# Kernel optimization log

Measured on AMD Instinct MI355X. Metric: run time of the kernel, lower is better.

## Reference

```python
import jax, jax.numpy as jnp
import numpy as np

B, L, E, H, D = 2, 4096, 512, 8, 64
DIL, WIN, CAUSAL = 2, 256, True
HID = 2048  # mlp_ratio * embed_dim
EPS = 1e-5


def _layernorm(x, g, b):
    mu = jnp.mean(x, axis=-1, keepdims=True)
    var = jnp.var(x, axis=-1, keepdims=True)
    return (x - mu) * jax.lax.rsqrt(var + EPS) * g + b


def _dilated_mask(Lq):
    i = jnp.arange(Lq)[:, None]
    j = jnp.arange(Lq)[None, :]
    d = i - j
    allowed = (d % DIL) == 0
    allowed &= jnp.abs(d) <= WIN
    if CAUSAL:
        allowed &= j <= i
    return allowed  # [L, L] bool


def setup_inputs() -> dict:
    key = jax.random.key(0)
    ks = jax.random.split(key, 5)
    s = 0.02
    return {
        "x": jax.random.normal(ks[0], (B, L, E), jnp.float32),
        "ln1_g": jnp.ones((E,), jnp.float32),
        "ln1_b": jnp.zeros((E,), jnp.float32),
        "qkv_w": jax.random.normal(ks[1], (E, 3 * E), jnp.float32) * s,
        "qkv_b": jnp.zeros((3 * E,), jnp.float32),
        "out_w": jax.random.normal(ks[2], (E, E), jnp.float32) * s,
        "out_b": jnp.zeros((E,), jnp.float32),
        "ln2_g": jnp.ones((E,), jnp.float32),
        "ln2_b": jnp.zeros((E,), jnp.float32),
        "w1": jax.random.normal(ks[3], (E, HID), jnp.float32) * s,
        "b1": jnp.zeros((HID,), jnp.float32),
        "w2": jax.random.normal(ks[4], (HID, E), jnp.float32) * s,
        "b2": jnp.zeros((E,), jnp.float32),
    }


def reference(x, ln1_g, ln1_b, qkv_w, qkv_b, out_w, out_b, ln2_g, ln2_b, w1, b1, w2, b2):
    b, l, e = x.shape
    # --- attention sublayer (pre-norm) ---
    h = _layernorm(x, ln1_g, ln1_b)
    qkv = h @ qkv_w + qkv_b                      # [B, L, 3E]
    q, k, v = jnp.split(qkv, 3, axis=-1)
    q = q.reshape(b, l, H, D).transpose(0, 2, 1, 3)  # [B, H, L, D]
    k = k.reshape(b, l, H, D).transpose(0, 2, 1, 3)
    v = v.reshape(b, l, H, D).transpose(0, 2, 1, 3)
    scores = jnp.einsum("bhqd,bhkd->bhqk", q, k) / jnp.sqrt(jnp.asarray(D, x.dtype))
    mask = _dilated_mask(l)                      # [L, L] bool, dilation+window+causal
    scores = jnp.where(mask, scores, jnp.finfo(scores.dtype).min)
    attn = jax.nn.softmax(scores, axis=-1)
    o = jnp.einsum("bhqk,bhkd->bhqd", attn, v)   # [B, H, L, D]
    o = o.transpose(0, 2, 1, 3).reshape(b, l, e)
    x = x + (o @ out_w + out_b)                  # dropout p=0
    # --- FFN sublayer (pre-norm) ---
    h2 = _layernorm(x, ln2_g, ln2_b)
    f = jax.nn.gelu(h2 @ w1 + b1, approximate=False) @ w2 + b2
    return x + f
```

## Files before the change

kernel.cpp:

```cpp
#include <hip/hip_runtime.h>
#include <math.h>

typedef unsigned char u8;
typedef unsigned short u16;
typedef unsigned int u32;
typedef __attribute__((ext_vector_type(4))) float f32x4;
typedef __attribute__((ext_vector_type(8))) short short8;

#define B_DIM 2
#define L_SEQ 4096
#define E_DIM 512
#define NH 8
#define HD 64
#define HID_DIM 2048
#define BL (B_DIM * L_SEQ)

__device__ __forceinline__ float bf2f(u16 u) {
    union { u32 i; float f; } v; v.i = ((u32)u) << 16; return v.f;
}
__device__ __forceinline__ u16 f2bf(float f) {
    union { float f; u32 i; } v; v.f = f;
    u32 r = v.i + 0x7fffu + ((v.i >> 16) & 1u);
    return (u16)(r >> 16);
}
__device__ __forceinline__ u32 pk2_fp8(float a, float b) {
    return (u32)__builtin_amdgcn_cvt_pk_fp8_f32(a, b, 0, false);
}
__device__ __forceinline__ u8 f2fp8(float a) { return (u8)(pk2_fp8(a, a) & 0xffu); }
__device__ __forceinline__ float gelu_f(float v) {
    float y = fminf(0.7978845608f * (v + 0.044715f * v * v * v), 15.f);
    float t = __expf(2.f * y);
    return v * (t / (t + 1.f));
}

#define GLOAD_LDS16(gp, lp) __builtin_amdgcn_global_load_lds( \
    (const __attribute__((address_space(1))) void*)(gp),      \
    (__attribute__((address_space(3))) void*)(lp), 16, 0, 0)

template<int VM> __device__ __forceinline__ void waitvm() {
    asm volatile("s_waitcnt vmcnt(%0)" :: "n"(VM) : "memory");
}

__global__ __launch_bounds__(256) void wconv_f8(const float* __restrict__ in,
                                                u8* __restrict__ out, int Kd, int Nd) {
    __shared__ u8 t[64][96];
    const int k0 = blockIdx.y * 64, n0 = blockIdx.x * 64;
    const int tid = threadIdx.x;
    const int col4 = tid & 15, rowb = tid >> 4;
#pragma unroll
    for (int i = 0; i < 4; ++i) {
        const int k = rowb + i * 16;
        const float4 v = *(const float4*)(in + (size_t)(k0 + k) * Nd + n0 + col4 * 4);
        const u32 p01 = pk2_fp8(v.x * 32.f, v.y * 32.f);
        const u32 p23 = pk2_fp8(v.z * 32.f, v.w * 32.f);
        t[col4 * 4 + 0][k] = (u8)(p01 & 0xff);
        t[col4 * 4 + 1][k] = (u8)((p01 >> 8) & 0xff);
        t[col4 * 4 + 2][k] = (u8)(p23 & 0xff);
        t[col4 * 4 + 3][k] = (u8)((p23 >> 8) & 0xff);
    }
    __syncthreads();
    const int n = tid >> 2, ch = tid & 3;
    u8* dst = out + (size_t)(n0 + n) * Kd + k0 + ch * 16;
    *(short8*)dst = *(const short8*)&t[n][ch * 16];
}

__global__ __launch_bounds__(256) void ln_f8(const float* __restrict__ x,
                                             const float* __restrict__ g,
                                             const float* __restrict__ b,
                                             u8* __restrict__ out) {
    const int row = blockIdx.x * 4 + (threadIdx.x >> 6);
    const int lane = threadIdx.x & 63;
    const float4* xr = (const float4*)(x + (size_t)row * E_DIM);
    const float4 v0 = xr[lane];
    const float4 v1 = xr[lane + 64];
    float s  = v0.x + v0.y + v0.z + v0.w + v1.x + v1.y + v1.z + v1.w;
    float s2 = v0.x*v0.x + v0.y*v0.y + v0.z*v0.z + v0.w*v0.w
             + v1.x*v1.x + v1.y*v1.y + v1.z*v1.z + v1.w*v1.w;
#pragma unroll
    for (int off = 32; off > 0; off >>= 1) {
        s  += __shfl_xor(s, off);
        s2 += __shfl_xor(s2, off);
    }
    const float mu = s * (1.f / E_DIM);
    const float rs = rsqrtf(s2 * (1.f / E_DIM) - mu * mu + 1e-5f);
    const float4 g0 = ((const float4*)g)[lane], g1 = ((const float4*)g)[lane + 64];
    const float4 b0 = ((const float4*)b)[lane], b1 = ((const float4*)b)[lane + 64];
    const float a0 = (v0.x - mu) * rs * g0.x + b0.x;
    const float a1 = (v0.y - mu) * rs * g0.y + b0.y;
    const float a2 = (v0.z - mu) * rs * g0.z + b0.z;
    const float a3 = (v0.w - mu) * rs * g0.w + b0.w;
    const float a4 = (v1.x - mu) * rs * g1.x + b1.x;
    const float a5 = (v1.y - mu) * rs * g1.y + b1.y;
    const float a6 = (v1.z - mu) * rs * g1.z + b1.z;
    const float a7 = (v1.w - mu) * rs * g1.w + b1.w;
    u32* orow = (u32*)(out + (size_t)row * E_DIM);
    orow[lane]      = pk2_fp8(a0, a1) | (pk2_fp8(a2, a3) << 16);
    orow[lane + 64] = pk2_fp8(a4, a5) | (pk2_fp8(a6, a7) << 16);
}

template<int K_T, int BN_T, int OUT, bool RES, bool GELU>
__global__ __launch_bounds__(512) void gemm_f8(const u8* __restrict__ A,
                                               const u8* __restrict__ Bt,
                                               const float* __restrict__ bias,
                                               const float* __restrict__ res,
                                               void* __restrict__ Cp,
                                               int M, int N, int nbx) {
    constexpr int K = K_T;
    constexpr int NT = K / 64;
    constexpr int MR = 4;
    constexpr int NR = BN_T / 64;
    constexpr int GA = 8;
    constexpr int GB = BN_T / 16;
    constexpr int LB = GB / 8;
    constexpr int L = 1 + LB;
    constexpr int AKG_S = GA * 256;
    constexpr int BKG_S = GB * 256;
    constexpr int ABYTES = 128 * 64;
    constexpr int BBYTES = BN_T * 64;
    constexpr int TILE = ABYTES + BBYTES;
    __shared__ u8 sb[3 * TILE];
    const int tid = threadIdx.x;
    const int wave = tid >> 6, lane = tid & 63;
    const int wr = wave >> 2, wc = wave & 3;

    const int xcd = blockIdx.x & 7;
    const int q = blockIdx.x >> 3;
    const int bx = q % nbx;
    const int by = (q / nbx) * 8 + xcd;
    const int bm = by * 128, bn = bx * BN_T;

    f32x4 acc[MR][NR];
#pragma unroll
    for (int m = 0; m < MR; ++m)
#pragma unroll
        for (int n = 0; n < NR; ++n) acc[m][n] = 0.f;

    const int lrow = (lane >> 4) * 16 + (lane & 15);

    auto stage = [&](int buf, int t) {
        u8* dst0 = sb + buf * TILE;
        {
            const int kg = wave >> 1, j = wave & 1;
            const u8* src = A + (size_t)(bm + j * 64 + lrow) * K
                            + t * 64 + (kg >> 1) * 32 + (kg & 1) * 16;
            GLOAD_LDS16(src, dst0 + kg * AKG_S + j * 1024);
        }
#pragma unroll
        for (int h = 0; h < LB; ++h) {
            const int i = wave * LB + h;
            const int kg = i / (GB / 4), j = i % (GB / 4);
            const u8* src = Bt + (size_t)(bn + j * 64 + lrow) * K
                            + t * 64 + (kg >> 1) * 32 + (kg & 1) * 16;
            GLOAD_LDS16(src, dst0 + ABYTES + kg * BKG_S + j * 1024);
        }
    };

    auto compute = [&](int buf) {
        const u8* base = sb + buf * TILE;
        const int g = lane >> 4, r = lane & 15;
        const int sub = g >> 1, off8 = (g & 1) * 8;
#pragma unroll
        for (int ks = 0; ks < 2; ++ks) {
            long av[MR], bv[NR];
#pragma unroll
            for (int m = 0; m < MR; ++m)
                av[m] = *(const long*)(base + (ks * 2 + sub) * AKG_S
                                       + (wr * 4 + m) * 256 + r * 16 + off8);
#pragma unroll
            for (int n = 0; n < NR; ++n)
                bv[n] = *(const long*)(base + ABYTES + (ks * 2 + sub) * BKG_S
                                       + (wc * NR + n) * 256 + r * 16 + off8);
            __builtin_amdgcn_s_setprio(1);
#pragma unroll
            for (int m = 0; m < MR; ++m)
#pragma unroll
                for (int n = 0; n < NR; ++n)
                    acc[m][n] = __builtin_amdgcn_mfma_f32_16x16x32_fp8_fp8(av[m], bv[n], acc[m][n], 0, 0, 0);
            __builtin_amdgcn_s_setprio(0);
        }
    };

    stage(0, 0);
    stage(1, 1);
    int sbuf = 2, cbuf = 0;
    for (int t = 0; t < NT - 2; ++t) {
        stage(sbuf, t + 2);
        sbuf = (sbuf == 2) ? 0 : sbuf + 1;
        waitvm<2 * L>();
        __builtin_amdgcn_s_barrier();
        compute(cbuf);
        cbuf = (cbuf == 2) ? 0 : cbuf + 1;
        __builtin_amdgcn_s_barrier();
    }
    waitvm<L>();
    __builtin_amdgcn_s_barrier();
    compute(cbuf);
    cbuf = (cbuf == 2) ? 0 : cbuf + 1;
    __builtin_amdgcn_s_barrier();
    waitvm<0>();
    __builtin_amdgcn_s_barrier();
    compute(cbuf);

    const int ccol = lane & 15;
    const int crow = (lane >> 4) * 4;
#pragma unroll
    for (int n = 0; n < NR; ++n) {
        const int gc = bn + wc * (NR * 16) + n * 16 + ccol;
        const float bi = bias[gc];
#pragma unroll
        for (int m = 0; m < MR; ++m) {
            const int gr0 = bm + wr * 64 + m * 16 + crow;
#pragma unroll
            for (int j = 0; j < 4; ++j) {
                float v = acc[m][n][j] * 0.03125f + bi;
                if (GELU) v = gelu_f(v);
                const size_t idx = (size_t)(gr0 + j) * N + gc;
                if (RES) v += res[idx];
                if (OUT == 0)      ((u16*)Cp)[idx] = f2bf(v);
                else if (OUT == 1) ((float*)Cp)[idx] = v;
                else               ((u8*)Cp)[idx] = f2fp8(v);
            }
        }
    }
}

__global__ __launch_bounds__(256) void attn_mfma(const u16* __restrict__ qkv,
                                                 u8* __restrict__ o) {
    __shared__ u16 K_lds[32 * 64];
    __shared__ u16 V_lds[32 * 64];
    const int tid = threadIdx.x;
    const int w = tid >> 6, lane = tid & 63;
    const int g = lane >> 4, q = lane & 15;
    const int qt = blockIdx.x, bph = blockIdx.y;
    const int b = bph >> 4, p = (bph >> 3) & 1, h = bph & 7;
    const int q0 = qt * 64;

    const size_t rowstride = 3 * E_DIM;
    const u16* qbase = qkv + (size_t)b * L_SEQ * rowstride + h * HD;

    const int qmin = q0 + w * 16, qmax = qmin + 15;
    const int qs_lane = qmin + q;
    const int qi = 2 * qs_lane + p;

    short8 qfrag[2];
    qfrag[0] = *(const short8*)(qbase + (size_t)qi * rowstride + g * 8);
    qfrag[1] = *(const short8*)(qbase + (size_t)qi * rowstride + 32 + g * 8);

    f32x4 oacc[4];
#pragma unroll
    for (int dt = 0; dt < 4; ++dt) oacc[dt] = 0.f;
    float m = -1e30f, l = 0.f;

    for (int s = 0; s < 6; ++s) {
        const int ks0 = q0 - 128 + 32 * s;
        if (ks0 >= 0) {
            const int r = 8 * w + (lane >> 3);
            const int gr = lane & 7;
            const size_t krow = (size_t)(2 * (ks0 + r) + p) * rowstride;
            const u16* ksrc = qbase + krow + E_DIM + 8 * (gr ^ (r & 7));
            const u16* vsrc = qbase + krow + 2 * E_DIM + 8 * gr;
            GLOAD_LDS16(ksrc, &K_lds[w * 512]);
            GLOAD_LDS16(vsrc, &V_lds[w * 512]);
        }
        __syncthreads();
        const bool active = (ks0 >= 0) && (ks0 <= qmax) && (ks0 + 31 >= qmin - 128);
        if (active) {
            f32x4 st[2];
            st[0] = 0.f; st[1] = 0.f;
#pragma unroll
            for (int t = 0; t < 2; ++t) {
#pragma unroll
                for (int c = 0; c < 2; ++c) {
                    const int kk = t * 16 + q;
                    const int gs = (c * 4 + g) ^ (kk & 7);
                    short8 kf = *(const short8*)&K_lds[kk * 64 + gs * 8];
                    st[t] = __builtin_amdgcn_mfma_f32_16x16x32_bf16(kf, qfrag[c], st[t], 0, 0, 0);
                }
            }
            float sv[2][4];
            float bm = -3.0e38f;
#pragma unroll
            for (int t = 0; t < 2; ++t)
#pragma unroll
                for (int j = 0; j < 4; ++j) {
                    const int kk = ks0 + t * 16 + 4 * g + j;
                    float x = st[t][j] * 0.125f;
                    const bool ok = (kk <= qs_lane) && (qs_lane - kk <= 128);
                    x = ok ? x : -3.0e38f;
                    sv[t][j] = x;
                    bm = fmaxf(bm, x);
                }
            bm = fmaxf(bm, __shfl_xor(bm, 16));
            bm = fmaxf(bm, __shfl_xor(bm, 32));
            const float mn = fmaxf(m, bm);
            const float sc = __expf(m - mn);
            m = mn;
            float rs = 0.f;
            u32 pk[2][2];
#pragma unroll
            for (int t = 0; t < 2; ++t) {
                const float e0 = __expf(sv[t][0] - mn), e1 = __expf(sv[t][1] - mn);
                const float e2 = __expf(sv[t][2] - mn), e3 = __expf(sv[t][3] - mn);
                rs += (e0 + e1) + (e2 + e3);
                pk[t][0] = (u32)f2bf(e0) | ((u32)f2bf(e1) << 16);
                pk[t][1] = (u32)f2bf(e2) | ((u32)f2bf(e3) << 16);
            }
            rs += __shfl_xor(rs, 16);
            rs += __shfl_xor(rs, 32);
            l = l * sc + rs;
#pragma unroll
            for (int dt = 0; dt < 4; ++dt) oacc[dt] *= sc;
            union { u32 w4[4]; short8 s8; } bfr;
#pragma unroll
            for (int r = 0; r < 4; ++r) {
                const int src = (((g << 1) + (r >> 1)) & 3) * 16 + q;
                const int w0 = __shfl((int)pk[0][r & 1], src);
                const int w1 = __shfl((int)pk[1][r & 1], src);
                bfr.w4[r] = (g & 2) ? (u32)w1 : (u32)w0;
            }
#pragma unroll
            for (int dt = 0; dt < 4; ++dt) {
                union { u16 h8[8]; short8 s8; } vf;
#pragma unroll
                for (int e = 0; e < 8; ++e)
                    vf.h8[e] = V_lds[(8 * g + e) * 64 + dt * 16 + q];
                oacc[dt] = __builtin_amdgcn_mfma_f32_16x16x32_bf16(vf.s8, bfr.s8, oacc[dt], 0, 0, 0);
            }
        }
        __syncthreads();
    }
    const float inv = 1.f / l;
    u8* obase = o + ((size_t)(b * L_SEQ) + (size_t)qi) * E_DIM + h * HD;
#pragma unroll
    for (int dt = 0; dt < 4; ++dt) {
        const u32 pw = pk2_fp8(oacc[dt][0] * inv, oacc[dt][1] * inv)
                     | (pk2_fp8(oacc[dt][2] * inv, oacc[dt][3] * inv) << 16);
        *(u32*)(obase + dt * 16 + 4 * g) = pw;
    }
}

extern "C" void kernel_launch(void* const* d_in, const int* in_sizes, int n_in,
                              void* d_out, int out_size, void* d_ws, size_t ws_size,
                              hipStream_t stream) {
    const float* x    = (const float*)d_in[0];
    const float* ln1g = (const float*)d_in[1];
    const float* ln1b = (const float*)d_in[2];
    const float* qkvw = (const float*)d_in[3];
    const float* qkvb = (const float*)d_in[4];
    const float* outw = (const float*)d_in[5];
    const float* outb = (const float*)d_in[6];
    const float* ln2g = (const float*)d_in[7];
    const float* ln2b = (const float*)d_in[8];
    const float* w1   = (const float*)d_in[9];
    const float* b1   = (const float*)d_in[10];
    const float* w2   = (const float*)d_in[11];
    const float* b2   = (const float*)d_in[12];
    float* outp = (float*)d_out;

    char* ws = (char*)d_ws;
    size_t off = 0;
    auto alloc = [&](size_t bytes) {
        void* p = ws + off;
        off += (bytes + 255) & ~(size_t)255;
        return p;
    };
    u8*    hbuf  = (u8*)   alloc((size_t)BL * E_DIM);
    u16*   qkvB  = (u16*)  alloc((size_t)BL * 3 * E_DIM * 2);
    u8*    obuf  = (u8*)   alloc((size_t)BL * E_DIM);
    float* x2    = (float*)alloc((size_t)BL * E_DIM * 4);
    u8*    h2    = (u8*)   alloc((size_t)BL * E_DIM);
    u8*    g1    = (u8*)   alloc((size_t)BL * HID_DIM);
    u8*    wqkvT = (u8*)   alloc((size_t)3 * E_DIM * E_DIM);
    u8*    woutT = (u8*)   alloc((size_t)E_DIM * E_DIM);
    u8*    w1T   = (u8*)   alloc((size_t)HID_DIM * E_DIM);
    u8*    w2T   = (u8*)   alloc((size_t)E_DIM * HID_DIM);

    wconv_f8<<<dim3((3 * E_DIM) / 64, E_DIM / 64), 256, 0, stream>>>(qkvw, wqkvT, E_DIM, 3 * E_DIM);
    wconv_f8<<<dim3(E_DIM / 64, E_DIM / 64), 256, 0, stream>>>(outw, woutT, E_DIM, E_DIM);
    wconv_f8<<<dim3(HID_DIM / 64, E_DIM / 64), 256, 0, stream>>>(w1, w1T, E_DIM, HID_DIM);
    wconv_f8<<<dim3(E_DIM / 64, HID_DIM / 64), 256, 0, stream>>>(w2, w2T, HID_DIM, E_DIM);

    ln_f8<<<BL / 4, 256, 0, stream>>>(x, ln1g, ln1b, hbuf);
    gemm_f8<E_DIM, 256, 0, false, false><<<(BL / 128) * 6, 512, 0, stream>>>(
        hbuf, wqkvT, qkvb, nullptr, qkvB, BL, 3 * E_DIM, 6);
    attn_mfma<<<dim3(32, 32), 256, 0, stream>>>(qkvB, obuf);
    gemm_f8<E_DIM, 128, 1, true, false><<<(BL / 128) * 4, 512, 0, stream>>>(
        obuf, woutT, outb, x, x2, BL, E_DIM, 4);
    ln_f8<<<BL / 4, 256, 0, stream>>>(x2, ln2g, ln2b, h2);
    gemm_f8<E_DIM, 256, 2, false, true><<<(BL / 128) * 8, 512, 0, stream>>>(
        h2, w1T, b1, nullptr, g1, BL, HID_DIM, 8);
    gemm_f8<HID_DIM, 128, 1, true, false><<<(BL / 128) * 4, 512, 0, stream>>>(
        g1, w2T, b2, x2, outp, BL, E_DIM, 4);
}
```

Measured before the change: 134.3 us.

## Fuse weight conversion with LN1, store residual in bf16, deepen 128-wide GEMM pipeline

Merges the four weight-conversion launches and the first layernorm into one prep kernel to cut launch overhead. The intermediate residual x2 is stored as bf16 instead of fp32, which halves its write and read traffic in the out-proj GEMM, LN2 and the final GEMM. The GEMMs with 128-wide N tiles use a 4-buffer LDS pipeline with a deeper prefetch instead of 3 buffers. The bf16 residual loses some precision in the skip connection, and the larger LDS footprint may lower occupancy.

```diff
diff --git a/kernel.cpp b/kernel.cpp
--- a/kernel.cpp
+++ b/kernel.cpp
@@ -41,11 +41,57 @@
     asm volatile("s_waitcnt vmcnt(%0)" :: "n"(VM) : "memory");
 }
 
-__global__ __launch_bounds__(256) void wconv_f8(const float* __restrict__ in,
-                                                u8* __restrict__ out, int Kd, int Nd) {
+__global__ __launch_bounds__(256) void prep(const float* __restrict__ qkvw,
+                                            const float* __restrict__ outw,
+                                            const float* __restrict__ w1,
+                                            const float* __restrict__ w2,
+                                            u8* __restrict__ wqkvT, u8* __restrict__ woutT,
+                                            u8* __restrict__ w1T, u8* __restrict__ w2T,
+                                            const float* __restrict__ x,
+                                            const float* __restrict__ g,
+                                            const float* __restrict__ b,
+                                            u8* __restrict__ hbuf) {
     __shared__ u8 t[64][96];
-    const int k0 = blockIdx.y * 64, n0 = blockIdx.x * 64;
+    int bid = blockIdx.x;
     const int tid = threadIdx.x;
+    if (bid < BL / 4) {
+        const int row = bid * 4 + (tid >> 6);
+        const int lane = tid & 63;
+        const float4* xr = (const float4*)(x + (size_t)row * E_DIM);
+        const float4 v0 = xr[lane];
+        const float4 v1 = xr[lane + 64];
+        float s  = v0.x + v0.y + v0.z + v0.w + v1.x + v1.y + v1.z + v1.w;
+        float s2 = v0.x*v0.x + v0.y*v0.y + v0.z*v0.z + v0.w*v0.w
+                 + v1.x*v1.x + v1.y*v1.y + v1.z*v1.z + v1.w*v1.w;
+#pragma unroll
+        for (int off = 32; off > 0; off >>= 1) {
+            s  += __shfl_xor(s, off);
+            s2 += __shfl_xor(s2, off);
+        }
+        const float mu = s * (1.f / E_DIM);
+        const float rs = rsqrtf(s2 * (1.f / E_DIM) - mu * mu + 1e-5f);
+        const float4 g0 = ((const float4*)g)[lane], g1 = ((const float4*)g)[lane + 64];
+        const float4 b0 = ((const float4*)b)[lane], b1 = ((const float4*)b)[lane + 64];
+        const float a0 = (v0.x - mu) * rs * g0.x + b0.x;
+        const float a1 = (v0.y - mu) * rs * g0.y + b0.y;
+        const float a2 = (v0.z - mu) * rs * g0.z + b0.z;
+        const float a3 = (v0.w - mu) * rs * g0.w + b0.w;
+        const float a4 = (v1.x - mu) * rs * g1.x + b1.x;
+        const float a5 = (v1.y - mu) * rs * g1.y + b1.y;
+        const float a6 = (v1.z - mu) * rs * g1.z + b1.z;
+        const float a7 = (v1.w - mu) * rs * g1.w + b1.w;
+        u32* orow = (u32*)(hbuf + (size_t)row * E_DIM);
+        orow[lane]      = pk2_fp8(a0, a1) | (pk2_fp8(a2, a3) << 16);
+        orow[lane + 64] = pk2_fp8(a4, a5) | (pk2_fp8(a6, a7) << 16);
+        return;
+    }
+    bid -= BL / 4;
+    const float* in; u8* out; int Kd, Nd, nbx;
+    if (bid < 192)      {            in = qkvw; out = wqkvT; Kd = E_DIM;   Nd = 3 * E_DIM; nbx = 24; }
+    else if (bid < 256) { bid -= 192; in = outw; out = woutT; Kd = E_DIM;   Nd = E_DIM;     nbx = 8;  }
+    else if (bid < 512) { bid -= 256; in = w1;   out = w1T;   Kd = E_DIM;   Nd = HID_DIM;   nbx = 32; }
+    else                { bid -= 512; in = w2;   out = w2T;   Kd = HID_DIM; Nd = E_DIM;     nbx = 8;  }
+    const int k0 = (bid / nbx) * 64, n0 = (bid % nbx) * 64;
     const int col4 = tid & 15, rowb = tid >> 4;
 #pragma unroll
     for (int i = 0; i < 4; ++i) {
@@ -64,18 +110,19 @@
     *(short8*)dst = *(const short8*)&t[n][ch * 16];
 }
 
-__global__ __launch_bounds__(256) void ln_f8(const float* __restrict__ x,
-                                             const float* __restrict__ g,
-                                             const float* __restrict__ b,
-                                             u8* __restrict__ out) {
+__global__ __launch_bounds__(256) void ln_b(const u16* __restrict__ x,
+                                            const float* __restrict__ g,
+                                            const float* __restrict__ b,
+                                            u8* __restrict__ out) {
     const int row = blockIdx.x * 4 + (threadIdx.x >> 6);
     const int lane = threadIdx.x & 63;
-    const float4* xr = (const float4*)(x + (size_t)row * E_DIM);
-    const float4 v0 = xr[lane];
-    const float4 v1 = xr[lane + 64];
-    float s  = v0.x + v0.y + v0.z + v0.w + v1.x + v1.y + v1.z + v1.w;
-    float s2 = v0.x*v0.x + v0.y*v0.y + v0.z*v0.z + v0.w*v0.w
-             + v1.x*v1.x + v1.y*v1.y + v1.z*v1.z + v1.w*v1.w;
+    const short8 v = *(const short8*)(x + (size_t)row * E_DIM + lane * 8);
+    float f[8];
+#pragma unroll
+    for (int j = 0; j < 8; ++j) f[j] = bf2f((u16)v[j]);
+    float s = 0.f, s2 = 0.f;
+#pragma unroll
+    for (int j = 0; j < 8; ++j) { s += f[j]; s2 += f[j] * f[j]; }
 #pragma unroll
     for (int off = 32; off > 0; off >>= 1) {
         s  += __shfl_xor(s, off);
@@ -83,26 +130,28 @@
     }
     const float mu = s * (1.f / E_DIM);
     const float rs = rsqrtf(s2 * (1.f / E_DIM) - mu * mu + 1e-5f);
-    const float4 g0 = ((const float4*)g)[lane], g1 = ((const float4*)g)[lane + 64];
-    const float4 b0 = ((const float4*)b)[lane], b1 = ((const float4*)b)[lane + 64];
-    const float a0 = (v0.x - mu) * rs * g0.x + b0.x;
-    const float a1 = (v0.y - mu) * rs * g0.y + b0.y;
-    const float a2 = (v0.z - mu) * rs * g0.z + b0.z;
-    const float a3 = (v0.w - mu) * rs * g0.w + b0.w;
-    const float a4 = (v1.x - mu) * rs * g1.x + b1.x;
-    const float a5 = (v1.y - mu) * rs * g1.y + b1.y;
-    const float a6 = (v1.z - mu) * rs * g1.z + b1.z;
-    const float a7 = (v1.w - mu) * rs * g1.w + b1.w;
-    u32* orow = (u32*)(out + (size_t)row * E_DIM);
-    orow[lane]      = pk2_fp8(a0, a1) | (pk2_fp8(a2, a3) << 16);
-    orow[lane + 64] = pk2_fp8(a4, a5) | (pk2_fp8(a6, a7) << 16);
-}
-
-template<int K_T, int BN_T, int OUT, bool RES, bool GELU>
+    const float4 g0 = ((const float4*)g)[lane * 2], g1 = ((const float4*)g)[lane * 2 + 1];
+    const float4 b0 = ((const float4*)b)[lane * 2], b1 = ((const float4*)b)[lane * 2 + 1];
+    float a[8];
+    a[0] = (f[0] - mu) * rs * g0.x + b0.x;
+    a[1] = (f[1] - mu) * rs * g0.y + b0.y;
+    a[2] = (f[2] - mu) * rs * g0.z + b0.z;
+    a[3] = (f[3] - mu) * rs * g0.w + b0.w;
+    a[4] = (f[4] - mu) * rs * g1.x + b1.x;
+    a[5] = (f[5] - mu) * rs * g1.y + b1.y;
+    a[6] = (f[6] - mu) * rs * g1.z + b1.z;
+    a[7] = (f[7] - mu) * rs * g1.w + b1.w;
+    uint2 pw;
+    pw.x = pk2_fp8(a[0], a[1]) | (pk2_fp8(a[2], a[3]) << 16);
+    pw.y = pk2_fp8(a[4], a[5]) | (pk2_fp8(a[6], a[7]) << 16);
+    *(uint2*)(out + (size_t)row * E_DIM + lane * 8) = pw;
+}
+
+template<int K_T, int BN_T, int OUT, int RESV, bool GELU>
 __global__ __launch_bounds__(512) void gemm_f8(const u8* __restrict__ A,
                                                const u8* __restrict__ Bt,
                                                const float* __restrict__ bias,
-                                               const float* __restrict__ res,
+                                               const void* __restrict__ resv,
                                                void* __restrict__ Cp,
                                                int M, int N, int nbx) {
     constexpr int K = K_T;
@@ -118,7 +167,8 @@
     constexpr int ABYTES = 128 * 64;
     constexpr int BBYTES = BN_T * 64;
     constexpr int TILE = ABYTES + BBYTES;
-    __shared__ u8 sb[3 * TILE];
+    constexpr int NBUF = (BN_T == 128) ? 4 : 3;
+    __shared__ u8 sb[NBUF * TILE];
     const int tid = threadIdx.x;
     const int wave = tid >> 6, lane = tid & 63;
     const int wr = wave >> 2, wc = wave & 3;
@@ -180,26 +230,50 @@
         }
     };
 
-    stage(0, 0);
-    stage(1, 1);
-    int sbuf = 2, cbuf = 0;
-    for (int t = 0; t < NT - 2; ++t) {
-        stage(sbuf, t + 2);
-        sbuf = (sbuf == 2) ? 0 : sbuf + 1;
+    if constexpr (BN_T == 128) {
+        stage(0, 0);
+        stage(1, 1);
+        stage(2, 2);
+        for (int t = 0; t < NT - 3; ++t) {
+            stage((t + 3) & 3, t + 3);
+            waitvm<3 * L>();
+            __builtin_amdgcn_s_barrier();
+            compute(t & 3);
+            __builtin_amdgcn_s_barrier();
+        }
         waitvm<2 * L>();
+        __builtin_amdgcn_s_barrier();
+        compute((NT - 3) & 3);
+        __builtin_amdgcn_s_barrier();
+        waitvm<L>();
+        __builtin_amdgcn_s_barrier();
+        compute((NT - 2) & 3);
+        __builtin_amdgcn_s_barrier();
+        waitvm<0>();
+        __builtin_amdgcn_s_barrier();
+        compute((NT - 1) & 3);
+    } else {
+        stage(0, 0);
+        stage(1, 1);
+        int sbuf = 2, cbuf = 0;
+        for (int t = 0; t < NT - 2; ++t) {
+            stage(sbuf, t + 2);
+            sbuf = (sbuf == 2) ? 0 : sbuf + 1;
+            waitvm<2 * L>();
+            __builtin_amdgcn_s_barrier();
+            compute(cbuf);
+            cbuf = (cbuf == 2) ? 0 : cbuf + 1;
+            __builtin_amdgcn_s_barrier();
+        }
+        waitvm<L>();
         __builtin_amdgcn_s_barrier();
         compute(cbuf);
         cbuf = (cbuf == 2) ? 0 : cbuf + 1;
         __builtin_amdgcn_s_barrier();
-    }
-    waitvm<L>();
-    __builtin_amdgcn_s_barrier();
-    compute(cbuf);
-    cbuf = (cbuf == 2) ? 0 : cbuf + 1;
-    __builtin_amdgcn_s_barrier();
-    waitvm<0>();
-    __builtin_amdgcn_s_barrier();
-    compute(cbuf);
+        waitvm<0>();
+        __builtin_amdgcn_s_barrier();
+        compute(cbuf);
+    }
 
     const int ccol = lane & 15;
     const int crow = (lane >> 4) * 4;
@@ -215,7 +289,8 @@
                 float v = acc[m][n][j] * 0.03125f + bi;
                 if (GELU) v = gelu_f(v);
                 const size_t idx = (size_t)(gr0 + j) * N + gc;
-                if (RES) v += res[idx];
+                if (RESV == 1)      v += ((const float*)resv)[idx];
+                else if (RESV == 2) v += bf2f(((const u16*)resv)[idx]);
                 if (OUT == 0)      ((u16*)Cp)[idx] = f2bf(v);
                 else if (OUT == 1) ((float*)Cp)[idx] = v;
                 else               ((u8*)Cp)[idx] = f2fp8(v);
@@ -367,7 +442,7 @@
     u8*    hbuf  = (u8*)   alloc((size_t)BL * E_DIM);
     u16*   qkvB  = (u16*)  alloc((size_t)BL * 3 * E_DIM * 2);
     u8*    obuf  = (u8*)   alloc((size_t)BL * E_DIM);
-    float* x2    = (float*)alloc((size_t)BL * E_DIM * 4);
+    u16*   x2    = (u16*)  alloc((size_t)BL * E_DIM * 2);
     u8*    h2    = (u8*)   alloc((size_t)BL * E_DIM);
     u8*    g1    = (u8*)   alloc((size_t)BL * HID_DIM);
     u8*    wqkvT = (u8*)   alloc((size_t)3 * E_DIM * E_DIM);
@@ -375,20 +450,16 @@
     u8*    w1T   = (u8*)   alloc((size_t)HID_DIM * E_DIM);
     u8*    w2T   = (u8*)   alloc((size_t)E_DIM * HID_DIM);
 
-    wconv_f8<<<dim3((3 * E_DIM) / 64, E_DIM / 64), 256, 0, stream>>>(qkvw, wqkvT, E_DIM, 3 * E_DIM);
-    wconv_f8<<<dim3(E_DIM / 64, E_DIM / 64), 256, 0, stream>>>(outw, woutT, E_DIM, E_DIM);
-    wconv_f8<<<dim3(HID_DIM / 64, E_DIM / 64), 256, 0, stream>>>(w1, w1T, E_DIM, HID_DIM);
-    wconv_f8<<<dim3(E_DIM / 64, HID_DIM / 64), 256, 0, stream>>>(w2, w2T, HID_DIM, E_DIM);
-
-    ln_f8<<<BL / 4, 256, 0, stream>>>(x, ln1g, ln1b, hbuf);
-    gemm_f8<E_DIM, 256, 0, false, false><<<(BL / 128) * 6, 512, 0, stream>>>(
+    prep<<<BL / 4 + 768, 256, 0, stream>>>(qkvw, outw, w1, w2, wqkvT, woutT, w1T, w2T,
+                                           x, ln1g, ln1b, hbuf);
+    gemm_f8<E_DIM, 256, 0, 0, false><<<(BL / 128) * 6, 512, 0, stream>>>(
         hbuf, wqkvT, qkvb, nullptr, qkvB, BL, 3 * E_DIM, 6);
     attn_mfma<<<dim3(32, 32), 256, 0, stream>>>(qkvB, obuf);
-    gemm_f8<E_DIM, 128, 1, true, false><<<(BL / 128) * 4, 512, 0, stream>>>(
+    gemm_f8<E_DIM, 128, 0, 1, false><<<(BL / 128) * 4, 512, 0, stream>>>(
         obuf, woutT, outb, x, x2, BL, E_DIM, 4);
-    ln_f8<<<BL / 4, 256, 0, stream>>>(x2, ln2g, ln2b, h2);
-    gemm_f8<E_DIM, 256, 2, false, true><<<(BL / 128) * 8, 512, 0, stream>>>(
+    ln_b<<<BL / 4, 256, 0, stream>>>(x2, ln2g, ln2b, h2);
+    gemm_f8<E_DIM, 256, 2, 0, true><<<(BL / 128) * 8, 512, 0, stream>>>(
         h2, w1T, b1, nullptr, g1, BL, HID_DIM, 8);
-    gemm_f8<HID_DIM, 128, 1, true, false><<<(BL / 128) * 4, 512, 0, stream>>>(
+    gemm_f8<HID_DIM, 128, 1, 2, false><<<(BL / 128) * 4, 512, 0, stream>>>(
         g1, w2T, b2, x2, outp, BL, E_DIM, 4);
 }
```

After: 121.9 us. 1.1x faster.
